# Kernel tuning notes

Hardware: AMD Instinct MI355X
Metric: run time of the kernel (lower is better)

Reference implementation:

```python
import jax, jax.numpy as jnp
import numpy as np

MARGIN = 1.0
EPS = 1e-6  # matches torch F.pairwise_distance eps added to the difference

def setup_inputs() -> dict:
    key = jax.random.key(0)
    k1, k2 = jax.random.split(key)
    B, D = 4096, 768
    embeddings = jax.random.normal(k1, (B, D), dtype=jnp.float32)
    labels = jax.random.randint(k2, (B,), 0, 6, dtype=jnp.int64)
    return {"embeddings": embeddings, "labels": labels,
            "depression_idx": 1, "suicidal_idx": 2}

def reference(embeddings, labels, depression_idx, suicidal_idx):
    # masks over the batch for the two classes
    dep_mask = (labels == depression_idx).astype(embeddings.dtype)  # [B]
    sui_mask = (labels == suicidal_idx).astype(embeddings.dtype)    # [B]

    # torch pairwise_distance computes ||d - s + eps||_2; shift the left side.
    d = embeddings + EPS                                             # [B, D]
    s = embeddings                                                   # [B, D]
    # squared distances via ||d||^2 + ||s||^2 - 2 d.s (single GEMM)
    d2 = jnp.sum(d * d, axis=-1)                                     # [B]
    s2 = jnp.sum(s * s, axis=-1)                                     # [B]
    dist2 = d2[:, None] + s2[None, :] - 2.0 * (d @ s.T)              # [B, B]
    dist = jnp.sqrt(jnp.maximum(dist2, 1e-12))                       # [B, B]

    hinge = jnp.maximum(MARGIN - dist, 0.0)                          # clamp(min=0)
    pair_mask = dep_mask[:, None] * sui_mask[None, :]                # [B, B]
    total = jnp.sum(hinge * pair_mask)
    count = jnp.sum(pair_mask)
    # mean over (depression, suicidal) pairs; 0.0 if either class is empty
    return jnp.where(count > 0, total / jnp.maximum(count, 1.0),
                     jnp.zeros((), embeddings.dtype))
```

## Files before the change

kernel.cpp:

```cpp
#include <hip/hip_runtime.h>
#include <hip/hip_bf16.h>

#define DIM   768
#define KITER (DIM / 32)
#define EPSF  1e-6f
#define MAXB  4096
#define NPB   256

typedef __attribute__((ext_vector_type(4))) float f32x4;
typedef __attribute__((ext_vector_type(8))) short short8;
typedef __attribute__((ext_vector_type(4))) unsigned short ushort4_t;

#define OFF_D2A   64
#define OFF_S2B   (64 + 16384)
#define OFF_PART  (64 + 32768)
#define OFF_IDXA  (64 + 32768 + 4096)
#define OFF_IDXB  (OFF_IDXA + 16384)
#define OFF_BF    (OFF_IDXB + 16384)
#define NEED_COMP ((size_t)OFF_BF + 2ull * MAXB * DIM * 2ull)

__device__ __forceinline__ unsigned short f2bf(float f) {
    return __builtin_bit_cast(unsigned short, __float2bfloat16(f));
}

__device__ __forceinline__ float hinge_from_d2(float dist2) {
    float dist = sqrtf(fmaxf(dist2, 1e-12f));
    return fmaxf(1.0f - dist, 0.0f);
}

template <bool ADD_EPS>
__device__ __forceinline__ short8 load_frag(const float* __restrict__ p) {
    const float4 u = *reinterpret_cast<const float4*>(p);
    const float4 v = *reinterpret_cast<const float4*>(p + 4);
    short8 f;
    if constexpr (ADD_EPS) {
        f[0] = (short)f2bf(u.x + EPSF); f[1] = (short)f2bf(u.y + EPSF);
        f[2] = (short)f2bf(u.z + EPSF); f[3] = (short)f2bf(u.w + EPSF);
        f[4] = (short)f2bf(v.x + EPSF); f[5] = (short)f2bf(v.y + EPSF);
        f[6] = (short)f2bf(v.z + EPSF); f[7] = (short)f2bf(v.w + EPSF);
    } else {
        f[0] = (short)f2bf(u.x); f[1] = (short)f2bf(u.y);
        f[2] = (short)f2bf(u.z); f[3] = (short)f2bf(u.w);
        f[4] = (short)f2bf(v.x); f[5] = (short)f2bf(v.y);
        f[6] = (short)f2bf(v.z); f[7] = (short)f2bf(v.w);
    }
    return f;
}

__global__ void __launch_bounds__(1024)
k_classify(const int* __restrict__ labels,
           const int* __restrict__ depi, const int* __restrict__ suii,
           int* __restrict__ cnt,
           int* __restrict__ idxA, int* __restrict__ idxB, int nrows)
{
    __shared__ int wtot[16];
    const int tid = threadIdx.x, lane = tid & 63, wv = tid >> 6;
    const int dep = depi[0], sui = suii[0];
    int baseA = 0, baseB = 0;
    for (int chunk = 0; chunk < nrows; chunk += 4096) {
        const int r0 = chunk + tid * 4;
        int l[4];
        #pragma unroll
        for (int j = 0; j < 4; ++j)
            l[j] = (r0 + j < nrows) ? labels[r0 + j] : 0x7fffffff;
        int ac = 0, bc = 0;
        #pragma unroll
        for (int j = 0; j < 4; ++j) { ac += (l[j] == dep); bc += (l[j] == sui); }
        int incl = ac | (bc << 16);
        const int own = incl;
        #pragma unroll
        for (int off = 1; off < 64; off <<= 1) {
            int n = __shfl_up(incl, off);
            if (lane >= off) incl += n;
        }
        if (lane == 63) wtot[wv] = incl;
        __syncthreads();
        if (tid < 16) {
            int v = wtot[tid];
            #pragma unroll
            for (int off = 1; off < 16; off <<= 1) {
                int n = __shfl_up(v, off);
                if (tid >= off) v += n;
            }
            wtot[tid] = v;
        }
        __syncthreads();
        const int wbase = wv ? wtot[wv - 1] : 0;
        const int excl  = wbase + incl - own;
        int pA = baseA + (excl & 0xFFFF);
        int pB = baseB + (excl >> 16);
        #pragma unroll
        for (int j = 0; j < 4; ++j) {
            const int row = r0 + j;
            if (row < nrows) {
                if (l[j] == dep) idxA[pA++] = row;
                if (l[j] == sui) idxB[pB++] = row;
            }
        }
        const int tot = wtot[15];
        baseA += tot & 0xFFFF;
        baseB += tot >> 16;
        __syncthreads();
    }
    if (tid == 0) { cnt[0] = baseA; cnt[1] = baseB; }
}

template <bool COMP>
__global__ void k_norms(const float* __restrict__ emb,
                        const int* __restrict__ cnt,
                        const int* __restrict__ idxA, const int* __restrict__ idxB,
                        float* __restrict__ d2A, float* __restrict__ s2B,
                        unsigned short* __restrict__ Abf,
                        unsigned short* __restrict__ Bbf)
{
    const int w    = blockIdx.x * 4 + (threadIdx.x >> 6);
    const int lane = threadIdx.x & 63;
    const int nA = cnt[0], nB = cnt[1];
    bool isA; int p;
    if (w < nA)               { isA = true;  p = w; }
    else if (w - nA < nB)     { isA = false; p = w - nA; }
    else return;

    const int row = isA ? idxA[p] : idxB[p];
    const float* rp = emb + (size_t)row * DIM;
    float4 v[3];
    float acc = 0.f;
    #pragma unroll
    for (int c = 0; c < 3; ++c) {
        v[c] = *reinterpret_cast<const float4*>(rp + c * 256 + lane * 4);
        if (isA) { v[c].x += EPSF; v[c].y += EPSF; v[c].z += EPSF; v[c].w += EPSF; }
        acc += v[c].x * v[c].x + v[c].y * v[c].y + v[c].z * v[c].z + v[c].w * v[c].w;
    }
    #pragma unroll
    for (int off = 32; off; off >>= 1) acc += __shfl_xor(acc, off);
    if (lane == 0) { if (isA) d2A[p] = acc; else s2B[p] = acc; }
    if constexpr (COMP) {
        unsigned short* dst = (isA ? Abf : Bbf) + (size_t)p * DIM;
        #pragma unroll
        for (int c = 0; c < 3; ++c) {
            ushort4_t wd;
            wd[0] = f2bf(v[c].x); wd[1] = f2bf(v[c].y);
            wd[2] = f2bf(v[c].z); wd[3] = f2bf(v[c].w);
            *reinterpret_cast<ushort4_t*>(dst + c * 256 + lane * 4) = wd;
        }
    }
}

template <bool COMP>
__global__ void __launch_bounds__(256)
k_pairs(const float* __restrict__ emb,
        const int* __restrict__ cnt,
        const float* __restrict__ d2A, const float* __restrict__ s2B,
        const int* __restrict__ idxA, const int* __restrict__ idxB,
        const unsigned short* __restrict__ Abf,
        const unsigned short* __restrict__ Bbf,
        float* __restrict__ partials)
{
    __shared__ float wsum[4];
    const int nA = cnt[0], nB = cnt[1];
    const unsigned nTi = (unsigned)(nA + 31) >> 5;
    const unsigned nTj = (unsigned)(nB + 31) >> 5;
    const unsigned T   = nTi * nTj;
    const int tid = threadIdx.x, wv = tid >> 6, lane = tid & 63;
    const int r = lane & 15, kq = lane >> 4;
    float wacc = 0.f;

    for (unsigned t = blockIdx.x + wv * gridDim.x; t < T; t += gridDim.x * 4) {
        const unsigned ti = t / nTj;
        const unsigned tj = t - ti * nTj;
        const int a0 = (int)(ti << 5), b0 = (int)(tj << 5);
        const int ar0 = min(a0 + r,      nA - 1);
        const int ar1 = min(a0 + 16 + r, nA - 1);
        const int br0 = min(b0 + r,      nB - 1);
        const int br1 = min(b0 + 16 + r, nB - 1);
        f32x4 acc00 = {0.f,0.f,0.f,0.f}, acc01 = {0.f,0.f,0.f,0.f};
        f32x4 acc10 = {0.f,0.f,0.f,0.f}, acc11 = {0.f,0.f,0.f,0.f};

        if constexpr (COMP) {
            const short8* pa0 = reinterpret_cast<const short8*>(Abf + (size_t)ar0 * DIM) + kq;
            const short8* pa1 = reinterpret_cast<const short8*>(Abf + (size_t)ar1 * DIM) + kq;
            const short8* pb0 = reinterpret_cast<const short8*>(Bbf + (size_t)br0 * DIM) + kq;
            const short8* pb1 = reinterpret_cast<const short8*>(Bbf + (size_t)br1 * DIM) + kq;
            #pragma unroll 6
            for (int kk = 0; kk < KITER; ++kk) {
                const short8 fa0 = pa0[4 * kk], fa1 = pa1[4 * kk];
                const short8 fb0 = pb0[4 * kk], fb1 = pb1[4 * kk];
                acc00 = __builtin_amdgcn_mfma_f32_16x16x32_bf16(fa0, fb0, acc00, 0, 0, 0);
                acc01 = __builtin_amdgcn_mfma_f32_16x16x32_bf16(fa0, fb1, acc01, 0, 0, 0);
                acc10 = __builtin_amdgcn_mfma_f32_16x16x32_bf16(fa1, fb0, acc10, 0, 0, 0);
                acc11 = __builtin_amdgcn_mfma_f32_16x16x32_bf16(fa1, fb1, acc11, 0, 0, 0);
            }
        } else {
            const float* qa0 = emb + (size_t)idxA[ar0] * DIM + kq * 8;
            const float* qa1 = emb + (size_t)idxA[ar1] * DIM + kq * 8;
            const float* qb0 = emb + (size_t)idxB[br0] * DIM + kq * 8;
            const float* qb1 = emb + (size_t)idxB[br1] * DIM + kq * 8;
            #pragma unroll 3
            for (int kk = 0; kk < KITER; ++kk) {
                const short8 fa0 = load_frag<true >(qa0 + 32 * kk);
                const short8 fa1 = load_frag<true >(qa1 + 32 * kk);
                const short8 fb0 = load_frag<false>(qb0 + 32 * kk);
                const short8 fb1 = load_frag<false>(qb1 + 32 * kk);
                acc00 = __builtin_amdgcn_mfma_f32_16x16x32_bf16(fa0, fb0, acc00, 0, 0, 0);
                acc01 = __builtin_amdgcn_mfma_f32_16x16x32_bf16(fa0, fb1, acc01, 0, 0, 0);
                acc10 = __builtin_amdgcn_mfma_f32_16x16x32_bf16(fa1, fb0, acc10, 0, 0, 0);
                acc11 = __builtin_amdgcn_mfma_f32_16x16x32_bf16(fa1, fb1, acc11, 0, 0, 0);
            }
        }

        const int bc0 = b0 + r, bc1 = b0 + 16 + r;
        const float s20 = (bc0 < nB) ? s2B[bc0] : 0.f;
        const float s21 = (bc1 < nB) ? s2B[bc1] : 0.f;
        #pragma unroll
        for (int j = 0; j < 4; ++j) {
            const int arl = a0 + (kq << 2) + j;
            const int arh = arl + 16;
            const float d2l = (arl < nA) ? d2A[arl] : 0.f;
            const float d2h = (arh < nA) ? d2A[arh] : 0.f;
            if (arl < nA && bc0 < nB) wacc += hinge_from_d2(d2l + s20 - 2.f * acc00[j]);
            if (arl < nA && bc1 < nB) wacc += hinge_from_d2(d2l + s21 - 2.f * acc01[j]);
            if (arh < nA && bc0 < nB) wacc += hinge_from_d2(d2h + s20 - 2.f * acc10[j]);
            if (arh < nA && bc1 < nB) wacc += hinge_from_d2(d2h + s21 - 2.f * acc11[j]);
        }
    }

    #pragma unroll
    for (int off = 32; off; off >>= 1) wacc += __shfl_down(wacc, off);
    if (lane == 0) wsum[wv] = wacc;
    __syncthreads();
    if (tid == 0)
        partials[blockIdx.x] = wsum[0] + wsum[1] + wsum[2] + wsum[3];
}

__global__ void __launch_bounds__(NPB)
k_final(const float* __restrict__ partials, const int* __restrict__ cnt,
        float* __restrict__ out)
{
    __shared__ float sm[NPB];
    const int tid = threadIdx.x;
    sm[tid] = partials[tid];
    __syncthreads();
    for (int off = NPB / 2; off; off >>= 1) {
        if (tid < off) sm[tid] += sm[tid + off];
        __syncthreads();
    }
    if (tid == 0) {
        const long long c = (long long)cnt[0] * (long long)cnt[1];
        out[0] = (c > 0) ? sm[0] / (float)c : 0.f;
    }
}

extern "C" void kernel_launch(void* const* d_in, const int* in_sizes, int n_in,
                              void* d_out, int out_size, void* d_ws, size_t ws_size,
                              hipStream_t stream)
{
    const float* emb  = (const float*)d_in[0];
    const int* labels = (const int*)d_in[1];
    const int* depi   = (const int*)d_in[2];
    const int* suii   = (const int*)d_in[3];
    float* out        = (float*)d_out;

    char* ws = (char*)d_ws;
    int*   cnt      = (int*)ws;
    float* d2A      = (float*)(ws + OFF_D2A);
    float* s2B      = (float*)(ws + OFF_S2B);
    float* partials = (float*)(ws + OFF_PART);
    int*   idxA     = (int*)(ws + OFF_IDXA);
    int*   idxB     = (int*)(ws + OFF_IDXB);
    unsigned short* Abf = (unsigned short*)(ws + OFF_BF);
    unsigned short* Bbf = Abf + (size_t)MAXB * DIM;

    const int nrows = in_sizes[0] / DIM;

    k_classify<<<1, 1024, 0, stream>>>(labels, depi, suii, cnt, idxA, idxB, nrows);
    const int nblk = (2 * nrows + 3) / 4;
    if (ws_size >= NEED_COMP) {
        k_norms<true><<<nblk, 256, 0, stream>>>(emb, cnt, idxA, idxB, d2A, s2B, Abf, Bbf);
        k_pairs<true><<<NPB, 256, 0, stream>>>(emb, cnt, d2A, s2B, idxA, idxB, Abf, Bbf, partials);
    } else {
        k_norms<false><<<nblk, 256, 0, stream>>>(emb, cnt, idxA, idxB, d2A, s2B, Abf, Bbf);
        k_pairs<false><<<NPB, 256, 0, stream>>>(emb, cnt, d2A, s2B, idxA, idxB, Abf, Bbf, partials);
    }
    k_final<<<1, NPB, 0, stream>>>(partials, cnt, out);
}
```

Before: 26.79 us.

## Fuse label classification into norm kernel via per-row prefix counts

Removes the single-block classify kernel and its launch. Each warp in the norms kernel now computes its compaction position by counting matching labels in all preceding rows, and the last row's warp writes the class counts. This trades one serial launch for redundant label scans whose cost grows with row index, O(B^2/64) loads, mostly served from cache.

```diff
diff --git a/kernel.cpp b/kernel.cpp
--- a/kernel.cpp
+++ b/kernel.cpp
@@ -47,101 +47,86 @@
     return f;
 }
 
-__global__ void __launch_bounds__(1024)
-k_classify(const int* __restrict__ labels,
-           const int* __restrict__ depi, const int* __restrict__ suii,
-           int* __restrict__ cnt,
-           int* __restrict__ idxA, int* __restrict__ idxB, int nrows)
-{
-    __shared__ int wtot[16];
-    const int tid = threadIdx.x, lane = tid & 63, wv = tid >> 6;
-    const int dep = depi[0], sui = suii[0];
-    int baseA = 0, baseB = 0;
-    for (int chunk = 0; chunk < nrows; chunk += 4096) {
-        const int r0 = chunk + tid * 4;
-        int l[4];
-        #pragma unroll
-        for (int j = 0; j < 4; ++j)
-            l[j] = (r0 + j < nrows) ? labels[r0 + j] : 0x7fffffff;
-        int ac = 0, bc = 0;
-        #pragma unroll
-        for (int j = 0; j < 4; ++j) { ac += (l[j] == dep); bc += (l[j] == sui); }
-        int incl = ac | (bc << 16);
-        const int own = incl;
-        #pragma unroll
-        for (int off = 1; off < 64; off <<= 1) {
-            int n = __shfl_up(incl, off);
-            if (lane >= off) incl += n;
-        }
-        if (lane == 63) wtot[wv] = incl;
-        __syncthreads();
-        if (tid < 16) {
-            int v = wtot[tid];
-            #pragma unroll
-            for (int off = 1; off < 16; off <<= 1) {
-                int n = __shfl_up(v, off);
-                if (tid >= off) v += n;
-            }
-            wtot[tid] = v;
-        }
-        __syncthreads();
-        const int wbase = wv ? wtot[wv - 1] : 0;
-        const int excl  = wbase + incl - own;
-        int pA = baseA + (excl & 0xFFFF);
-        int pB = baseB + (excl >> 16);
-        #pragma unroll
-        for (int j = 0; j < 4; ++j) {
-            const int row = r0 + j;
-            if (row < nrows) {
-                if (l[j] == dep) idxA[pA++] = row;
-                if (l[j] == sui) idxB[pB++] = row;
-            }
-        }
-        const int tot = wtot[15];
-        baseA += tot & 0xFFFF;
-        baseB += tot >> 16;
-        __syncthreads();
-    }
-    if (tid == 0) { cnt[0] = baseA; cnt[1] = baseB; }
-}
-
 template <bool COMP>
 __global__ void k_norms(const float* __restrict__ emb,
-                        const int* __restrict__ cnt,
-                        const int* __restrict__ idxA, const int* __restrict__ idxB,
+                        const int* __restrict__ labels,
+                        const int* __restrict__ depi,
+                        const int* __restrict__ suii,
+                        int* __restrict__ cnt,
+                        int* __restrict__ idxA, int* __restrict__ idxB,
                         float* __restrict__ d2A, float* __restrict__ s2B,
                         unsigned short* __restrict__ Abf,
-                        unsigned short* __restrict__ Bbf)
-{
-    const int w    = blockIdx.x * 4 + (threadIdx.x >> 6);
+                        unsigned short* __restrict__ Bbf, int nrows)
+{
+    const int row  = blockIdx.x * 4 + (threadIdx.x >> 6);
     const int lane = threadIdx.x & 63;
-    const int nA = cnt[0], nB = cnt[1];
-    bool isA; int p;
-    if (w < nA)               { isA = true;  p = w; }
-    else if (w - nA < nB)     { isA = false; p = w - nA; }
-    else return;
-
-    const int row = isA ? idxA[p] : idxB[p];
+    if (row >= nrows) return;
+    const int dep = depi[0], sui = suii[0];
+    const int lab = labels[row];
+    const bool isA = (lab == dep), isB = (lab == sui);
+    const bool isLast = (row == nrows - 1);
+    if (!(isA | isB) && !isLast) return;
+
+    int packed = 0;
+    for (int j = lane; j < row; j += 64) {
+        const int l = labels[j];
+        packed += (l == dep) + ((l == sui) << 16);
+    }
+    #pragma unroll
+    for (int off = 32; off; off >>= 1) packed += __shfl_xor(packed, off);
+    const int pA = packed & 0xFFFF;
+    const int pB = packed >> 16;
+    if (isLast && lane == 0) {
+        cnt[0] = pA + (isA ? 1 : 0);
+        cnt[1] = pB + (isB ? 1 : 0);
+    }
+    if (!(isA | isB)) return;
+
     const float* rp = emb + (size_t)row * DIM;
     float4 v[3];
-    float acc = 0.f;
+    float s2 = 0.f, d2 = 0.f;
     #pragma unroll
     for (int c = 0; c < 3; ++c) {
         v[c] = *reinterpret_cast<const float4*>(rp + c * 256 + lane * 4);
-        if (isA) { v[c].x += EPSF; v[c].y += EPSF; v[c].z += EPSF; v[c].w += EPSF; }
-        acc += v[c].x * v[c].x + v[c].y * v[c].y + v[c].z * v[c].z + v[c].w * v[c].w;
-    }
-    #pragma unroll
-    for (int off = 32; off; off >>= 1) acc += __shfl_xor(acc, off);
-    if (lane == 0) { if (isA) d2A[p] = acc; else s2B[p] = acc; }
-    if constexpr (COMP) {
-        unsigned short* dst = (isA ? Abf : Bbf) + (size_t)p * DIM;
-        #pragma unroll
-        for (int c = 0; c < 3; ++c) {
-            ushort4_t wd;
-            wd[0] = f2bf(v[c].x); wd[1] = f2bf(v[c].y);
-            wd[2] = f2bf(v[c].z); wd[3] = f2bf(v[c].w);
-            *reinterpret_cast<ushort4_t*>(dst + c * 256 + lane * 4) = wd;
+        s2 += v[c].x * v[c].x + v[c].y * v[c].y + v[c].z * v[c].z + v[c].w * v[c].w;
+        const float dx = v[c].x + EPSF, dy = v[c].y + EPSF;
+        const float dz = v[c].z + EPSF, dw = v[c].w + EPSF;
+        d2 += dx * dx + dy * dy + dz * dz + dw * dw;
+    }
+    int pk2 = __builtin_bit_cast(int, s2);
+    float d2r = d2;
+    #pragma unroll
+    for (int off = 32; off; off >>= 1) {
+        pk2 = __builtin_bit_cast(int,
+              __builtin_bit_cast(float, pk2) + __shfl_xor(__builtin_bit_cast(float, pk2), off));
+        d2r += __shfl_xor(d2r, off);
+    }
+    const float s2t = __builtin_bit_cast(float, pk2);
+
+    if (isA) {
+        if (lane == 0) { d2A[pA] = d2r; idxA[pA] = row; }
+        if constexpr (COMP) {
+            unsigned short* dst = Abf + (size_t)pA * DIM;
+            #pragma unroll
+            for (int c = 0; c < 3; ++c) {
+                ushort4_t wd;
+                wd[0] = f2bf(v[c].x + EPSF); wd[1] = f2bf(v[c].y + EPSF);
+                wd[2] = f2bf(v[c].z + EPSF); wd[3] = f2bf(v[c].w + EPSF);
+                *reinterpret_cast<ushort4_t*>(dst + c * 256 + lane * 4) = wd;
+            }
+        }
+    }
+    if (isB) {
+        if (lane == 0) { s2B[pB] = s2t; idxB[pB] = row; }
+        if constexpr (COMP) {
+            unsigned short* dst = Bbf + (size_t)pB * DIM;
+            #pragma unroll
+            for (int c = 0; c < 3; ++c) {
+                ushort4_t wd;
+                wd[0] = f2bf(v[c].x); wd[1] = f2bf(v[c].y);
+                wd[2] = f2bf(v[c].z); wd[3] = f2bf(v[c].w);
+                *reinterpret_cast<ushort4_t*>(dst + c * 256 + lane * 4) = wd;
+            }
         }
     }
 }
@@ -271,15 +256,18 @@
     unsigned short* Bbf = Abf + (size_t)MAXB * DIM;
 
     const int nrows = in_sizes[0] / DIM;
-
-    k_classify<<<1, 1024, 0, stream>>>(labels, depi, suii, cnt, idxA, idxB, nrows);
-    const int nblk = (2 * nrows + 3) / 4;
+    const int nblk  = (nrows + 3) / 4;
+
     if (ws_size >= NEED_COMP) {
-        k_norms<true><<<nblk, 256, 0, stream>>>(emb, cnt, idxA, idxB, d2A, s2B, Abf, Bbf);
-        k_pairs<true><<<NPB, 256, 0, stream>>>(emb, cnt, d2A, s2B, idxA, idxB, Abf, Bbf, partials);
+        k_norms<true><<<nblk, 256, 0, stream>>>(emb, labels, depi, suii, cnt,
+                                                idxA, idxB, d2A, s2B, Abf, Bbf, nrows);
+        k_pairs<true><<<NPB, 256, 0, stream>>>(emb, cnt, d2A, s2B, idxA, idxB,
+                                               Abf, Bbf, partials);
     } else {
-        k_norms<false><<<nblk, 256, 0, stream>>>(emb, cnt, idxA, idxB, d2A, s2B, Abf, Bbf);
-        k_pairs<false><<<NPB, 256, 0, stream>>>(emb, cnt, d2A, s2B, idxA, idxB, Abf, Bbf, partials);
+        k_norms<false><<<nblk, 256, 0, stream>>>(emb, labels, depi, suii, cnt,
+                                                 idxA, idxB, d2A, s2B, Abf, Bbf, nrows);
+        k_pairs<false><<<NPB, 256, 0, stream>>>(emb, cnt, d2A, s2B, idxA, idxB,
+                                                Abf, Bbf, partials);
     }
     k_final<<<1, NPB, 0, stream>>>(partials, cnt, out);
 }
```

New measurement: 26.87 us. Within noise of the previous version (+0.3%).
